# Kernel optimization log

Hardware: AMD Instinct MI355X
Metric: run time of the kernel (lower is better)

## Reference

```python
import jax, jax.numpy as jnp
import numpy as np

EPS = 1e-8
TEMPERATURE = 1.0


def setup_inputs() -> dict:
    key = jax.random.key(0)
    k1, k2, k3 = jax.random.split(key, 3)
    B, Q, K, H, D = 64, 64, 8192, 1, 64
    return {
        "query": jax.random.normal(k1, (B, Q, H, D), dtype=jnp.float32),
        "key": jax.random.normal(k2, (B, K, H, D), dtype=jnp.float32),
        "value": jax.random.normal(k3, (B, K, H, D), dtype=jnp.float32),
    }


def reference(query, key, value):
    # InvertedDotProductAttention(norm_type='mean', multi_head=False)
    d = query.shape[-1]
    q = query / jnp.sqrt(jnp.asarray(d, query.dtype))
    # logits: [B, H, Q, K]
    attn = jnp.einsum("bqhd,bkhd->bhqk", q, key)
    # inverted attention: softmax over the QUERY axis (-2)
    attn = jax.nn.softmax(attn / TEMPERATURE, axis=-2)
    attn = jnp.clip(attn, 0.0, 1.0)
    # renormalize over keys (norm_type == 'mean')
    attn = attn / (jnp.sum(attn, axis=-1, keepdims=True) + EPS)
    out = jnp.einsum("bhqk,bkhd->bqhd", attn, value)
    # single-head: squeeze heads dim
    out = jnp.squeeze(out, axis=-2)          # [B, Q, Dv]
    attn_weights = jnp.squeeze(attn, axis=-3)  # [B, Q, K]
    return out, attn_weights
```

## Files before the change

kernel.cpp:

```cpp
#include <hip/hip_runtime.h>
#include <cstddef>

#define NB 64
#define NQ 64
#define NK 8192
#define ND 64
#define KPB 256
#define KSL 512
#define NSLICE (NK / KSL)

typedef __attribute__((ext_vector_type(8))) short short8_t;
typedef __attribute__((ext_vector_type(8))) unsigned short ushort8_t;
typedef __attribute__((ext_vector_type(4))) unsigned short ushort4_t;
typedef __attribute__((ext_vector_type(4))) float float4_t;

static __device__ __forceinline__ unsigned short f2bf(float f) {
    unsigned b = __float_as_uint(f);
    b += 0x7FFFu + ((b >> 16) & 1u);
    return (unsigned short)(b >> 16);
}
static __device__ __forceinline__ float bf2f(unsigned short u) {
    return __uint_as_float(((unsigned)u) << 16);
}
static __device__ __forceinline__ void split8(const float* f, short8_t& hi, short8_t& lo) {
#pragma unroll
    for (int j = 0; j < 8; ++j) {
        const unsigned u = __float_as_uint(f[j]);
        hi[j] = (short)(u >> 16);
        const float lof = f[j] - __uint_as_float(u & 0xFFFF0000u);
        lo[j] = (short)(__float_as_uint(lof) >> 16);
    }
}

__global__ __launch_bounds__(256, 3) void k_qk_p(
    const float* __restrict__ query,
    const float* __restrict__ key,
    unsigned short* __restrict__ pstore,
    float* __restrict__ rowsum)
{
    __shared__ alignas(16) unsigned short SH[64 * 264];
    unsigned short* Qhi = SH;
    unsigned short* Qlo = SH + 64 * 72;

    const int tid  = threadIdx.x;
    const int b    = blockIdx.y;
    const int k0   = blockIdx.x * KPB;
    const int lane = tid & 63;
    const int w    = tid >> 6;
    const int lq   = lane & 15;
    const int lg   = lane >> 4;

    const float* krb = key + ((size_t)b * NK + k0 + w * 64 + lq) * ND + lg * 8;

    float kfA[16], kfB[16];
#define LOADK(KF, S)                                                           \
    {                                                                          \
        const float* kr = krb + (size_t)(S) * 16 * ND;                         \
        *reinterpret_cast<float4*>(KF)      = *reinterpret_cast<const float4*>(kr);      \
        *reinterpret_cast<float4*>(KF + 4)  = *reinterpret_cast<const float4*>(kr + 4);  \
        *reinterpret_cast<float4*>(KF + 8)  = *reinterpret_cast<const float4*>(kr + 32); \
        *reinterpret_cast<float4*>(KF + 12) = *reinterpret_cast<const float4*>(kr + 36); \
    }

    LOADK(kfA, 0);
    LOADK(kfB, 1);

    {
        const float* qb = query + (size_t)b * NQ * ND;
#pragma unroll
        for (int i = 0; i < 2; ++i) {
            const int o  = tid + 256 * i;
            const int q  = o >> 3;
            const int d0 = (o & 7) * 8;
            float f[8];
            *reinterpret_cast<float4*>(f)     = *reinterpret_cast<const float4*>(qb + q * ND + d0);
            *reinterpret_cast<float4*>(f + 4) = *reinterpret_cast<const float4*>(qb + q * ND + d0 + 4);
            short8_t h, l8;
            split8(f, h, l8);
            const int n    = q >> 4;
            const int l    = (q & 15) | (((d0 >> 3) & 3) << 4);
            const int dh   = d0 >> 5;
            const int base = l * 72 + n * 16 + dh * 8;
            *reinterpret_cast<short8_t*>(&Qhi[base]) = h;
            *reinterpret_cast<short8_t*>(&Qlo[base]) = l8;
        }
    }
    __syncthreads();

    short8_t bhi[4][2], blo[4][2];
#pragma unroll
    for (int n = 0; n < 4; ++n)
#pragma unroll
        for (int dh = 0; dh < 2; ++dh) {
            const int base = lane * 72 + n * 16 + dh * 8;
            bhi[n][dh] = *reinterpret_cast<const short8_t*>(&Qhi[base]);
            blo[n][dh] = *reinterpret_cast<const short8_t*>(&Qlo[base]);
        }
    __syncthreads();

    unsigned short* pL = SH;
    float rsacc[4] = {0.f, 0.f, 0.f, 0.f};

#define DO_SUBTILE(S, KF, PRE)                                                 \
    {                                                                          \
        short8_t ahi[2], alo[2];                                               \
        split8(KF, ahi[0], alo[0]);                                            \
        split8(KF + 8, ahi[1], alo[1]);                                        \
        if ((PRE) < 4) LOADK(KF, PRE);        \
        float4_t acc[4];                                                       \
        _Pragma("unroll")                                                      \
        for (int n = 0; n < 4; ++n) acc[n] = (float4_t){0.f, 0.f, 0.f, 0.f};   \
        _Pragma("unroll")                                                      \
        for (int n = 0; n < 4; ++n)                                            \
            _Pragma("unroll")                                                  \
            for (int dh = 0; dh < 2; ++dh) {                                   \
                acc[n] = __builtin_amdgcn_mfma_f32_16x16x32_bf16(ahi[dh], bhi[n][dh], acc[n], 0, 0, 0); \
                acc[n] = __builtin_amdgcn_mfma_f32_16x16x32_bf16(ahi[dh], blo[n][dh], acc[n], 0, 0, 0); \
                acc[n] = __builtin_amdgcn_mfma_f32_16x16x32_bf16(alo[dh], bhi[n][dh], acc[n], 0, 0, 0); \
            }                                                                  \
        float z[4] = {0.f, 0.f, 0.f, 0.f};                                     \
        _Pragma("unroll")                                                      \
        for (int n = 0; n < 4; ++n)                                            \
            _Pragma("unroll")                                                  \
            for (int r = 0; r < 4; ++r) {                                      \
                acc[n][r] = __expf(acc[n][r] * 0.125f);      \
                z[r] += acc[n][r];                                             \
            }                                                                  \
        _Pragma("unroll")                                                      \
        for (int r = 0; r < 4; ++r) {                                          \
            z[r] += __shfl_xor(z[r], 1, 64);                                   \
            z[r] += __shfl_xor(z[r], 2, 64);                                   \
            z[r] += __shfl_xor(z[r], 4, 64);                                   \
            z[r] += __shfl_xor(z[r], 8, 64);                                   \
            z[r] = 1.f / z[r];                                                 \
        }                                                                      \
        _Pragma("unroll")                                                      \
        for (int n = 0; n < 4; ++n) {                                          \
            ushort4_t u;                                                       \
            float rs = 0.f;                                                    \
            _Pragma("unroll")                                                  \
            for (int r = 0; r < 4; ++r) {                                      \
                u[r] = f2bf(acc[n][r] * z[r]);             \
                rs += bf2f(u[r]);                                              \
            }                                                                  \
            *reinterpret_cast<ushort4_t*>(                                     \
                &pL[(16 * n + lq) * 264 + w * 64 + (S) * 16 + lg * 4]) = u;    \
            rs += __shfl_xor(rs, 16, 64);                                      \
            rs += __shfl_xor(rs, 32, 64);                                      \
            rsacc[n] += rs;                                                    \
        }                                                                      \
    }

    DO_SUBTILE(0, kfA, 2);
    DO_SUBTILE(1, kfB, 3);
    DO_SUBTILE(2, kfA, 4);
    DO_SUBTILE(3, kfB, 4);
#undef DO_SUBTILE
#undef LOADK

    if (lg == 0) {
#pragma unroll
        for (int n = 0; n < 4; ++n)
            atomicAdd(&rowsum[b * NQ + lq + 16 * n], rsacc[n]);
    }
    __syncthreads();

    {
        const int cl = tid & 63;
#pragma unroll
        for (int t = 0; t < 16; ++t) {
            const int row = t * 4 + w;
            const ushort4_t u = *reinterpret_cast<const ushort4_t*>(&pL[row * 264 + cl * 4]);
            const int c      = cl * 4;
            const int half   = c >> 7;
            const int slot   = (c & 127) >> 3;
            const int sub    = (c >> 2) & 1;
            const int sp     = slot ^ (row & 7);
            *reinterpret_cast<ushort4_t*>(pstore +
                ((size_t)(b * NQ + row)) * NK + k0 + half * 128 + sp * 8 + sub * 4) = u;
        }
    }
}

template<bool PART>
__global__ __launch_bounds__(256, 4) void k_scale_pv(
    const unsigned short* __restrict__ psrc,
    const float* __restrict__ value,
    const float* __restrict__ rowsum,
    float* __restrict__ attn,
    float* __restrict__ dst)
{
    __shared__ alignas(16) unsigned short pLu[64 * 128];
    __shared__ alignas(16) unsigned short Vsu[128 * 68];
    __shared__ float rsL[NQ];

    const int tid  = threadIdx.x;
    const int b    = blockIdx.y;
    const int ks   = blockIdx.x;
    const int k0   = ks * KSL;
    const int lane = tid & 63;
    const int w    = tid >> 6;
    const int lq   = lane & 15;
    const int lg   = lane >> 4;

    if (tid < NQ) rsL[tid] = 1.f / (rowsum[b * NQ + tid] + 1e-8f);

    const unsigned short* pg = psrc + (size_t)b * NQ * NK;
    const float4* vg = reinterpret_cast<const float4*>(value + ((size_t)b * NK + k0) * ND);

    ushort8_t rp[4];
    float4 rv[8];
#pragma unroll
    for (int i = 0; i < 4; ++i) {
        const int idx = tid + 256 * i;
        rp[i] = *reinterpret_cast<const ushort8_t*>(
            &pg[(size_t)(idx >> 4) * NK + k0 + (idx & 15) * 8]);
    }
#pragma unroll
    for (int i = 0; i < 8; ++i) rv[i] = vg[tid + 256 * i];

    float4_t oacc[4];
#pragma unroll
    for (int n = 0; n < 4; ++n) oacc[n] = (float4_t){0.f, 0.f, 0.f, 0.f};

#pragma unroll 1
    for (int ht = 0; ht < 4; ++ht) {
        __syncthreads();

#pragma unroll
        for (int i = 0; i < 4; ++i) {
            const int idx  = tid + 256 * i;
            const int row  = idx >> 4;
            const int sl   = idx & 15;
            const int slog = sl ^ (row & 7);
            const float iv = rsL[row];
            float f[8];
            ushort8_t u;
#pragma unroll
            for (int j = 0; j < 8; ++j) {
                f[j] = bf2f(rp[i][j]) * iv;
                u[j] = f2bf(f[j]);
            }
            float* ap = attn + ((size_t)(b * NQ + row)) * NK + k0 + ht * 128 + slog * 8;
            *reinterpret_cast<float4*>(ap)     = *reinterpret_cast<float4*>(f);
            *reinterpret_cast<float4*>(ap + 4) = *reinterpret_cast<float4*>(f + 4);
            *reinterpret_cast<ushort8_t*>(&pLu[idx * 8]) = u;
        }
#pragma unroll
        for (int i = 0; i < 8; ++i) {
            const int idx = tid + 256 * i;
            ushort4_t v4;
            v4[0] = f2bf(rv[i].x); v4[1] = f2bf(rv[i].y);
            v4[2] = f2bf(rv[i].z); v4[3] = f2bf(rv[i].w);
            *reinterpret_cast<ushort4_t*>(&Vsu[(idx >> 4) * 68 + (idx & 15) * 4]) = v4;
        }

        if (ht < 3) {
            const int kn = k0 + (ht + 1) * 128;
#pragma unroll
            for (int i = 0; i < 4; ++i) {
                const int idx = tid + 256 * i;
                rp[i] = *reinterpret_cast<const ushort8_t*>(
                    &pg[(size_t)(idx >> 4) * NK + kn + (idx & 15) * 8]);
            }
#pragma unroll
            for (int i = 0; i < 8; ++i)
                rv[i] = vg[(ht + 1) * 2048 + tid + 256 * i];
        }
        __syncthreads();

#pragma unroll
        for (int h = 0; h < 4; ++h) {
            short8_t vb;
#pragma unroll
            for (int j = 0; j < 8; ++j)
                vb[j] = (short)Vsu[(h * 32 + lg * 8 + j) * 68 + 16 * w + lq];
#pragma unroll
            for (int n = 0; n < 4; ++n) {
                const short8_t pa = *reinterpret_cast<const short8_t*>(
                    &pLu[(16 * n + lq) * 128 + (((h * 4 + lg) ^ (lq & 7)) * 8)]);
                oacc[n] = __builtin_amdgcn_mfma_f32_16x16x32_bf16(pa, vb, oacc[n], 0, 0, 0);
            }
        }
    }

    if (PART) {
        float* pb = dst + ((size_t)(b * NSLICE + ks)) * (NQ * ND);
#pragma unroll
        for (int n = 0; n < 4; ++n)
#pragma unroll
            for (int r = 0; r < 4; ++r)
                pb[(16 * n + 4 * lg + r) * ND + 16 * w + lq] = oacc[n][r];
    } else {
#pragma unroll
        for (int n = 0; n < 4; ++n)
#pragma unroll
            for (int r = 0; r < 4; ++r)
                atomicAdd(dst + ((size_t)(b * NQ + 16 * n + 4 * lg + r)) * ND + 16 * w + lq,
                          oacc[n][r]);
    }
}

__global__ __launch_bounds__(256) void k_reduce_out(
    const float* __restrict__ partials,
    float* __restrict__ out)
{
    const int b   = blockIdx.y;
    const int idx = blockIdx.x * 256 + threadIdx.x;
    const float4* pb = reinterpret_cast<const float4*>(partials + (size_t)b * NSLICE * NQ * ND);
    float4 sum = make_float4(0.f, 0.f, 0.f, 0.f);
#pragma unroll
    for (int s = 0; s < NSLICE; ++s) {
        const float4 v = pb[(size_t)s * (NQ * ND / 4) + idx];
        sum.x += v.x; sum.y += v.y; sum.z += v.z; sum.w += v.w;
    }
    reinterpret_cast<float4*>(out + (size_t)b * NQ * ND)[idx] = sum;
}

extern "C" void kernel_launch(void* const* d_in, const int* in_sizes, int n_in,
                              void* d_out, int out_size, void* d_ws, size_t ws_size,
                              hipStream_t stream) {
    const float* query = (const float*)d_in[0];
    const float* key   = (const float*)d_in[1];
    const float* value = (const float*)d_in[2];

    float* out  = (float*)d_out;
    float* attn = (float*)d_out + (size_t)NB * NQ * ND;

    const size_t PB_BYTES   = (size_t)NB * NQ * NK * sizeof(unsigned short);
    const size_t PART_BYTES = (size_t)NB * NSLICE * NQ * ND * sizeof(float);

    float* rowsum = (float*)d_ws;
    unsigned short* pbuf = (unsigned short*)((char*)d_ws + 16384);
    float* partials = (float*)((char*)d_ws + 16384 + PB_BYTES);
    const bool part = ws_size >= 16384 + PB_BYTES + PART_BYTES;

    hipMemsetAsync(rowsum, 0, (size_t)NB * NQ * sizeof(float), stream);
    if (!part)
        hipMemsetAsync(out, 0, (size_t)NB * NQ * ND * sizeof(float), stream);

    dim3 gA(NK / KPB, NB);
    k_qk_p<<<gA, 256, 0, stream>>>(query, key, pbuf, rowsum);

    dim3 gB(NK / KSL, NB);
    if (part) {
        k_scale_pv<true><<<gB, 256, 0, stream>>>(pbuf, value, rowsum, attn, partials);
        k_reduce_out<<<dim3(4, NB), 256, 0, stream>>>(partials, out);
    } else {
        k_scale_pv<false><<<gB, 256, 0, stream>>>(pbuf, value, rowsum, attn, out);
    }
}
```

Before: 118.4 us.

## Double-buffer P tiles and defer row normalization to the output reduction

The PV kernel now keeps two register buffers of P tiles and software-pipelines the four 128-key subtiles: it loads the next tile, stages the current one into shared memory, then runs the MFMAs while writing the attention output. Unnormalized bf16 P goes straight into the MFMA, and the 1/rowsum scaling moves to the partial-reduction kernel, or to a new normalize kernel on the atomic path. This drops the per-element bf16 re-rounding from the staging step and hoists the rowsum reads. The cost is more registers and one extra small kernel on the fallback path.

Measured after the change: 128.4 us. 8.4% more time.

```diff
diff --git a/kernel.cpp b/kernel.cpp
--- a/kernel.cpp
+++ b/kernel.cpp
@@ -106,7 +106,7 @@
         short8_t ahi[2], alo[2];                                               \
         split8(KF, ahi[0], alo[0]);                                            \
         split8(KF + 8, ahi[1], alo[1]);                                        \
-        if ((PRE) < 4) LOADK(KF, PRE);        \
+        if ((PRE) < 4) LOADK(KF, PRE);                                         \
         float4_t acc[4];                                                       \
         _Pragma("unroll")                                                      \
         for (int n = 0; n < 4; ++n) acc[n] = (float4_t){0.f, 0.f, 0.f, 0.f};   \
@@ -123,7 +123,7 @@
         for (int n = 0; n < 4; ++n)                                            \
             _Pragma("unroll")                                                  \
             for (int r = 0; r < 4; ++r) {                                      \
-                acc[n][r] = __expf(acc[n][r] * 0.125f);      \
+                acc[n][r] = __expf(acc[n][r] * 0.125f);                        \
                 z[r] += acc[n][r];                                             \
             }                                                                  \
         _Pragma("unroll")                                                      \
@@ -140,7 +140,7 @@
             float rs = 0.f;                                                    \
             _Pragma("unroll")                                                  \
             for (int r = 0; r < 4; ++r) {                                      \
-                u[r] = f2bf(acc[n][r] * z[r]);             \
+                u[r] = f2bf(acc[n][r] * z[r]);                                 \
                 rs += bf2f(u[r]);                                              \
             }                                                                  \
             *reinterpret_cast<ushort4_t*>(                                     \
@@ -208,81 +208,105 @@
     const unsigned short* pg = psrc + (size_t)b * NQ * NK;
     const float4* vg = reinterpret_cast<const float4*>(value + ((size_t)b * NK + k0) * ND);
 
-    ushort8_t rp[4];
+    ushort8_t rpA[4], rpB[4];
     float4 rv[8];
-#pragma unroll
-    for (int i = 0; i < 4; ++i) {
-        const int idx = tid + 256 * i;
-        rp[i] = *reinterpret_cast<const ushort8_t*>(
-            &pg[(size_t)(idx >> 4) * NK + k0 + (idx & 15) * 8]);
-    }
-#pragma unroll
-    for (int i = 0; i < 8; ++i) rv[i] = vg[tid + 256 * i];
+
+#define LOADP(RP, HT)                                                          \
+    {                                                                          \
+        _Pragma("unroll")                                                      \
+        for (int i = 0; i < 4; ++i) {                                          \
+            const int idx = tid + 256 * i;                                     \
+            RP[i] = *reinterpret_cast<const ushort8_t*>(                       \
+                &pg[(size_t)(idx >> 4) * NK + k0 + (HT) * 128 + (idx & 15) * 8]); \
+        }                                                                      \
+    }
+#define LOADV(HT)                                                              \
+    {                                                                          \
+        _Pragma("unroll")                                                      \
+        for (int i = 0; i < 8; ++i) rv[i] = vg[(HT) * 2048 + tid + 256 * i];   \
+    }
+#define STAGE(RP)                                                              \
+    {                                                                          \
+        _Pragma("unroll")                                                      \
+        for (int i = 0; i < 4; ++i)                                            \
+            *reinterpret_cast<ushort8_t*>(&pLu[(tid + 256 * i) * 8]) = RP[i];  \
+        _Pragma("unroll")                                                      \
+        for (int i = 0; i < 8; ++i) {                                          \
+            const int idx = tid + 256 * i;                                     \
+            ushort4_t v4;                                                      \
+            v4[0] = f2bf(rv[i].x); v4[1] = f2bf(rv[i].y);                      \
+            v4[2] = f2bf(rv[i].z); v4[3] = f2bf(rv[i].w);                      \
+            *reinterpret_cast<ushort4_t*>(&Vsu[(idx >> 4) * 68 + (idx & 15) * 4]) = v4; \
+        }                                                                      \
+    }
+#define PVATTN(RP, HT)                                                         \
+    {                                                                          \
+        _Pragma("unroll")                                                      \
+        for (int h = 0; h < 4; ++h) {                                          \
+            short8_t vb;                                                       \
+            _Pragma("unroll")                                                  \
+            for (int j = 0; j < 8; ++j)                                        \
+                vb[j] = (short)Vsu[(h * 32 + lg * 8 + j) * 68 + 16 * w + lq];  \
+            _Pragma("unroll")                                                  \
+            for (int n = 0; n < 4; ++n) {                                      \
+                const short8_t pa = *reinterpret_cast<const short8_t*>(        \
+                    &pLu[(16 * n + lq) * 128 + (((h * 4 + lg) ^ (lq & 7)) * 8)]); \
+                oacc[n] = __builtin_amdgcn_mfma_f32_16x16x32_bf16(pa, vb, oacc[n], 0, 0, 0); \
+            }                                                                  \
+        }                                                                      \
+        _Pragma("unroll")                                                      \
+        for (int i = 0; i < 4; ++i) {                                          \
+            const int idx  = tid + 256 * i;                                    \
+            const int row  = idx >> 4;                                         \
+            const int slog = (idx & 15) ^ (row & 7);                           \
+            float f[8];                                                        \
+            _Pragma("unroll")                                                  \
+            for (int j = 0; j < 8; ++j) f[j] = bf2f(RP[i][j]) * ivr[i];        \
+            float* ap = attn + ((size_t)(b * NQ + row)) * NK + k0 +            \
+                        (HT) * 128 + slog * 8;                                 \
+            *reinterpret_cast<float4*>(ap)     = *reinterpret_cast<float4*>(f);     \
+            *reinterpret_cast<float4*>(ap + 4) = *reinterpret_cast<float4*>(f + 4); \
+        }                                                                      \
+    }
 
     float4_t oacc[4];
 #pragma unroll
     for (int n = 0; n < 4; ++n) oacc[n] = (float4_t){0.f, 0.f, 0.f, 0.f};
 
-#pragma unroll 1
-    for (int ht = 0; ht < 4; ++ht) {
-        __syncthreads();
-
-#pragma unroll
-        for (int i = 0; i < 4; ++i) {
-            const int idx  = tid + 256 * i;
-            const int row  = idx >> 4;
-            const int sl   = idx & 15;
-            const int slog = sl ^ (row & 7);
-            const float iv = rsL[row];
-            float f[8];
-            ushort8_t u;
-#pragma unroll
-            for (int j = 0; j < 8; ++j) {
-                f[j] = bf2f(rp[i][j]) * iv;
-                u[j] = f2bf(f[j]);
-            }
-            float* ap = attn + ((size_t)(b * NQ + row)) * NK + k0 + ht * 128 + slog * 8;
-            *reinterpret_cast<float4*>(ap)     = *reinterpret_cast<float4*>(f);
-            *reinterpret_cast<float4*>(ap + 4) = *reinterpret_cast<float4*>(f + 4);
-            *reinterpret_cast<ushort8_t*>(&pLu[idx * 8]) = u;
-        }
-#pragma unroll
-        for (int i = 0; i < 8; ++i) {
-            const int idx = tid + 256 * i;
-            ushort4_t v4;
-            v4[0] = f2bf(rv[i].x); v4[1] = f2bf(rv[i].y);
-            v4[2] = f2bf(rv[i].z); v4[3] = f2bf(rv[i].w);
-            *reinterpret_cast<ushort4_t*>(&Vsu[(idx >> 4) * 68 + (idx & 15) * 4]) = v4;
-        }
-
-        if (ht < 3) {
-            const int kn = k0 + (ht + 1) * 128;
-#pragma unroll
-            for (int i = 0; i < 4; ++i) {
-                const int idx = tid + 256 * i;
-                rp[i] = *reinterpret_cast<const ushort8_t*>(
-                    &pg[(size_t)(idx >> 4) * NK + kn + (idx & 15) * 8]);
-            }
-#pragma unroll
-            for (int i = 0; i < 8; ++i)
-                rv[i] = vg[(ht + 1) * 2048 + tid + 256 * i];
-        }
-        __syncthreads();
-
-#pragma unroll
-        for (int h = 0; h < 4; ++h) {
-            short8_t vb;
-#pragma unroll
-            for (int j = 0; j < 8; ++j)
-                vb[j] = (short)Vsu[(h * 32 + lg * 8 + j) * 68 + 16 * w + lq];
-#pragma unroll
-            for (int n = 0; n < 4; ++n) {
-                const short8_t pa = *reinterpret_cast<const short8_t*>(
-                    &pLu[(16 * n + lq) * 128 + (((h * 4 + lg) ^ (lq & 7)) * 8)]);
-                oacc[n] = __builtin_amdgcn_mfma_f32_16x16x32_bf16(pa, vb, oacc[n], 0, 0, 0);
-            }
-        }
-    }
+    LOADP(rpA, 0);
+    LOADV(0);
+    __syncthreads();
+
+    float ivr[4];
+#pragma unroll
+    for (int i = 0; i < 4; ++i) ivr[i] = rsL[(tid + 256 * i) >> 4];
+
+    LOADP(rpB, 1);
+    STAGE(rpA);
+    LOADV(1);
+    __syncthreads();
+    PVATTN(rpA, 0);
+    __syncthreads();
+    LOADP(rpA, 2);
+    STAGE(rpB);
+    LOADV(2);
+    __syncthreads();
+    PVATTN(rpB, 1);
+    __syncthreads();
+    LOADP(rpB, 3);
+    STAGE(rpA);
+    LOADV(3);
+    __syncthreads();
+    PVATTN(rpA, 2);
+    __syncthreads();
+    STAGE(rpB);
+    __syncthreads();
+    PVATTN(rpB, 3);
+
+#undef LOADP
+#undef LOADV
+#undef STAGE
+#undef PVATTN
 
     if (PART) {
         float* pb = dst + ((size_t)(b * NSLICE + ks)) * (NQ * ND);
@@ -303,10 +327,13 @@
 
 __global__ __launch_bounds__(256) void k_reduce_out(
     const float* __restrict__ partials,
+    const float* __restrict__ rowsum,
     float* __restrict__ out)
 {
     const int b   = blockIdx.y;
     const int idx = blockIdx.x * 256 + threadIdx.x;
+    const int q   = idx >> 4;
+    const float iv = 1.f / (rowsum[b * NQ + q] + 1e-8f);
     const float4* pb = reinterpret_cast<const float4*>(partials + (size_t)b * NSLICE * NQ * ND);
     float4 sum = make_float4(0.f, 0.f, 0.f, 0.f);
 #pragma unroll
@@ -314,7 +341,22 @@
         const float4 v = pb[(size_t)s * (NQ * ND / 4) + idx];
         sum.x += v.x; sum.y += v.y; sum.z += v.z; sum.w += v.w;
     }
+    sum.x *= iv; sum.y *= iv; sum.z *= iv; sum.w *= iv;
     reinterpret_cast<float4*>(out + (size_t)b * NQ * ND)[idx] = sum;
+}
+
+__global__ __launch_bounds__(256) void k_norm_out(
+    const float* __restrict__ rowsum,
+    float* __restrict__ out)
+{
+    const int b   = blockIdx.y;
+    const int idx = blockIdx.x * 256 + threadIdx.x;
+    const int q   = idx >> 4;
+    const float iv = 1.f / (rowsum[b * NQ + q] + 1e-8f);
+    float4* op = reinterpret_cast<float4*>(out + (size_t)b * NQ * ND) + idx;
+    float4 v = *op;
+    v.x *= iv; v.y *= iv; v.z *= iv; v.w *= iv;
+    *op = v;
 }
 
 extern "C" void kernel_launch(void* const* d_in, const int* in_sizes, int n_in,
@@ -345,8 +387,9 @@
     dim3 gB(NK / KSL, NB);
     if (part) {
         k_scale_pv<true><<<gB, 256, 0, stream>>>(pbuf, value, rowsum, attn, partials);
-        k_reduce_out<<<dim3(4, NB), 256, 0, stream>>>(partials, out);
+        k_reduce_out<<<dim3(4, NB), 256, 0, stream>>>(partials, rowsum, out);
     } else {
         k_scale_pv<false><<<gB, 256, 0, stream>>>(pbuf, value, rowsum, attn, out);
-    }
-}
+        k_norm_out<<<dim3(4, NB), 256, 0, stream>>>(rowsum, out);
+    }
+}
```

## Split attn scaling from PV, defer row normalization to the output reduction

Applied to the files above, without the earlier changes.

The PV kernel now multiplies the unnormalized bf16 probabilities by V directly. The per-row 1/rowsum factor is applied afterwards in the reduction kernel, using linearity. Writing the fp32 attention weights moves into a separate k_scale kernel that streams the bf16 buffer a second time. This drops the per-element scaling and fp32 stores from the MFMA kernel, but adds an extra launch and a re-read of the P buffer. The PV product also changes slightly, because it now uses unscaled bf16 P instead of re-rounded scaled P.

After: 132.6 us. +12.0%, slower.

```diff
diff --git a/kernel.cpp b/kernel.cpp
--- a/kernel.cpp
+++ b/kernel.cpp
@@ -106,7 +106,7 @@
         short8_t ahi[2], alo[2];                                               \
         split8(KF, ahi[0], alo[0]);                                            \
         split8(KF + 8, ahi[1], alo[1]);                                        \
-        if ((PRE) < 4) LOADK(KF, PRE);        \
+        if ((PRE) < 4) LOADK(KF, PRE);                                         \
         float4_t acc[4];                                                       \
         _Pragma("unroll")                                                      \
         for (int n = 0; n < 4; ++n) acc[n] = (float4_t){0.f, 0.f, 0.f, 0.f};   \
@@ -123,7 +123,7 @@
         for (int n = 0; n < 4; ++n)                                            \
             _Pragma("unroll")                                                  \
             for (int r = 0; r < 4; ++r) {                                      \
-                acc[n][r] = __expf(acc[n][r] * 0.125f);      \
+                acc[n][r] = __expf(acc[n][r] * 0.125f);                        \
                 z[r] += acc[n][r];                                             \
             }                                                                  \
         _Pragma("unroll")                                                      \
@@ -140,7 +140,7 @@
             float rs = 0.f;                                                    \
             _Pragma("unroll")                                                  \
             for (int r = 0; r < 4; ++r) {                                      \
-                u[r] = f2bf(acc[n][r] * z[r]);             \
+                u[r] = f2bf(acc[n][r] * z[r]);                                 \
                 rs += bf2f(u[r]);                                              \
             }                                                                  \
             *reinterpret_cast<ushort4_t*>(                                     \
@@ -183,16 +183,13 @@
 }
 
 template<bool PART>
-__global__ __launch_bounds__(256, 4) void k_scale_pv(
+__global__ __launch_bounds__(256, 4) void k_pv(
     const unsigned short* __restrict__ psrc,
     const float* __restrict__ value,
-    const float* __restrict__ rowsum,
-    float* __restrict__ attn,
     float* __restrict__ dst)
 {
     __shared__ alignas(16) unsigned short pLu[64 * 128];
     __shared__ alignas(16) unsigned short Vsu[128 * 68];
-    __shared__ float rsL[NQ];
 
     const int tid  = threadIdx.x;
     const int b    = blockIdx.y;
@@ -203,21 +200,29 @@
     const int lq   = lane & 15;
     const int lg   = lane >> 4;
 
-    if (tid < NQ) rsL[tid] = 1.f / (rowsum[b * NQ + tid] + 1e-8f);
-
     const unsigned short* pg = psrc + (size_t)b * NQ * NK;
     const float4* vg = reinterpret_cast<const float4*>(value + ((size_t)b * NK + k0) * ND);
 
     ushort8_t rp[4];
     float4 rv[8];
-#pragma unroll
-    for (int i = 0; i < 4; ++i) {
-        const int idx = tid + 256 * i;
-        rp[i] = *reinterpret_cast<const ushort8_t*>(
-            &pg[(size_t)(idx >> 4) * NK + k0 + (idx & 15) * 8]);
-    }
-#pragma unroll
-    for (int i = 0; i < 8; ++i) rv[i] = vg[tid + 256 * i];
+
+#define LOADP(HT)                                                              \
+    {                                                                          \
+        _Pragma("unroll")                                                      \
+        for (int i = 0; i < 4; ++i) {                                          \
+            const int idx = tid + 256 * i;                                     \
+            rp[i] = *reinterpret_cast<const ushort8_t*>(                       \
+                &pg[(size_t)(idx >> 4) * NK + k0 + (HT) * 128 + (idx & 15) * 8]); \
+        }                                                                      \
+    }
+#define LOADV(HT)                                                              \
+    {                                                                          \
+        _Pragma("unroll")                                                      \
+        for (int i = 0; i < 8; ++i) rv[i] = vg[(HT) * 2048 + tid + 256 * i];   \
+    }
+
+    LOADP(0);
+    LOADV(0);
 
     float4_t oacc[4];
 #pragma unroll
@@ -228,24 +233,8 @@
         __syncthreads();
 
 #pragma unroll
-        for (int i = 0; i < 4; ++i) {
-            const int idx  = tid + 256 * i;
-            const int row  = idx >> 4;
-            const int sl   = idx & 15;
-            const int slog = sl ^ (row & 7);
-            const float iv = rsL[row];
-            float f[8];
-            ushort8_t u;
-#pragma unroll
-            for (int j = 0; j < 8; ++j) {
-                f[j] = bf2f(rp[i][j]) * iv;
-                u[j] = f2bf(f[j]);
-            }
-            float* ap = attn + ((size_t)(b * NQ + row)) * NK + k0 + ht * 128 + slog * 8;
-            *reinterpret_cast<float4*>(ap)     = *reinterpret_cast<float4*>(f);
-            *reinterpret_cast<float4*>(ap + 4) = *reinterpret_cast<float4*>(f + 4);
-            *reinterpret_cast<ushort8_t*>(&pLu[idx * 8]) = u;
-        }
+        for (int i = 0; i < 4; ++i)
+            *reinterpret_cast<ushort8_t*>(&pLu[(tid + 256 * i) * 8]) = rp[i];
 #pragma unroll
         for (int i = 0; i < 8; ++i) {
             const int idx = tid + 256 * i;
@@ -256,16 +245,8 @@
         }
 
         if (ht < 3) {
-            const int kn = k0 + (ht + 1) * 128;
-#pragma unroll
-            for (int i = 0; i < 4; ++i) {
-                const int idx = tid + 256 * i;
-                rp[i] = *reinterpret_cast<const ushort8_t*>(
-                    &pg[(size_t)(idx >> 4) * NK + kn + (idx & 15) * 8]);
-            }
-#pragma unroll
-            for (int i = 0; i < 8; ++i)
-                rv[i] = vg[(ht + 1) * 2048 + tid + 256 * i];
+            LOADP(ht + 1);
+            LOADV(ht + 1);
         }
         __syncthreads();
 
@@ -283,6 +264,8 @@
             }
         }
     }
+#undef LOADP
+#undef LOADV
 
     if (PART) {
         float* pb = dst + ((size_t)(b * NSLICE + ks)) * (NQ * ND);
@@ -301,12 +284,45 @@
     }
 }
 
+__global__ __launch_bounds__(256) void k_scale(
+    const unsigned short* __restrict__ psrc,
+    const float* __restrict__ rowsum,
+    float* __restrict__ attn)
+{
+    const int b   = blockIdx.y;
+    const int row = blockIdx.x * 4 + (threadIdx.x >> 6);
+    const int cl  = threadIdx.x & 63;
+
+    const float iv = 1.f / (rowsum[b * NQ + row] + 1e-8f);
+    const unsigned short* pr = psrc + ((size_t)(b * NQ + row)) * NK;
+    float* ar = attn + ((size_t)(b * NQ + row)) * NK;
+    const int rx = row & 7;
+
+#pragma unroll
+    for (int it = 0; it < 16; ++it) {
+        const int idx  = it * 64 + cl;
+        const ushort8_t u = *reinterpret_cast<const ushort8_t*>(&pr[idx * 8]);
+        const int half = idx >> 4;
+        const int sp   = idx & 15;
+        const int slog = sp ^ rx;
+        float f[8];
+#pragma unroll
+        for (int j = 0; j < 8; ++j) f[j] = bf2f(u[j]) * iv;
+        float* dp = ar + half * 128 + slog * 8;
+        *reinterpret_cast<float4*>(dp)     = *reinterpret_cast<float4*>(f);
+        *reinterpret_cast<float4*>(dp + 4) = *reinterpret_cast<float4*>(f + 4);
+    }
+}
+
 __global__ __launch_bounds__(256) void k_reduce_out(
     const float* __restrict__ partials,
+    const float* __restrict__ rowsum,
     float* __restrict__ out)
 {
     const int b   = blockIdx.y;
     const int idx = blockIdx.x * 256 + threadIdx.x;
+    const int q   = idx >> 4;
+    const float iv = 1.f / (rowsum[b * NQ + q] + 1e-8f);
     const float4* pb = reinterpret_cast<const float4*>(partials + (size_t)b * NSLICE * NQ * ND);
     float4 sum = make_float4(0.f, 0.f, 0.f, 0.f);
 #pragma unroll
@@ -314,7 +330,22 @@
         const float4 v = pb[(size_t)s * (NQ * ND / 4) + idx];
         sum.x += v.x; sum.y += v.y; sum.z += v.z; sum.w += v.w;
     }
+    sum.x *= iv; sum.y *= iv; sum.z *= iv; sum.w *= iv;
     reinterpret_cast<float4*>(out + (size_t)b * NQ * ND)[idx] = sum;
+}
+
+__global__ __launch_bounds__(256) void k_norm_out(
+    const float* __restrict__ rowsum,
+    float* __restrict__ out)
+{
+    const int b   = blockIdx.y;
+    const int idx = blockIdx.x * 256 + threadIdx.x;
+    const int q   = idx >> 4;
+    const float iv = 1.f / (rowsum[b * NQ + q] + 1e-8f);
+    float4* op = reinterpret_cast<float4*>(out + (size_t)b * NQ * ND) + idx;
+    float4 v = *op;
+    v.x *= iv; v.y *= iv; v.z *= iv; v.w *= iv;
+    *op = v;
 }
 
 extern "C" void kernel_launch(void* const* d_in, const int* in_sizes, int n_in,
@@ -344,9 +375,12 @@
 
     dim3 gB(NK / KSL, NB);
     if (part) {
-        k_scale_pv<true><<<gB, 256, 0, stream>>>(pbuf, value, rowsum, attn, partials);
-        k_reduce_out<<<dim3(4, NB), 256, 0, stream>>>(partials, out);
+        k_pv<true><<<gB, 256, 0, stream>>>(pbuf, value, partials);
+        k_scale<<<dim3(NQ / 4, NB), 256, 0, stream>>>(pbuf, rowsum, attn);
+        k_reduce_out<<<dim3(4, NB), 256, 0, stream>>>(partials, rowsum, out);
     } else {
-        k_scale_pv<false><<<gB, 256, 0, stream>>>(pbuf, value, rowsum, attn, out);
-    }
-}
+        k_pv<false><<<gB, 256, 0, stream>>>(pbuf, value, out);
+        k_scale<<<dim3(NQ / 4, NB), 256, 0, stream>>>(pbuf, rowsum, attn);
+        k_norm_out<<<dim3(4, NB), 256, 0, stream>>>(rowsum, out);
+    }
+}
```
